# Optimization experiments

Hardware: AMD Instinct MI355X
Metric: run time of the kernel (lower is better)

Reference implementation:

```python
import jax, jax.numpy as jnp
import numpy as np

AVG_NOBJ = 49.0
NEG_SLOPE = 0.01  # torch leaky_relu default


def eops_1_to_2(x, nobj, aggregation):
    """x: [B,N,C] -> [B,C,5,N,N] equivariant basis (rank-1 -> rank-2)."""
    B, N, C = x.shape
    xt = jnp.transpose(x, (0, 2, 1))  # B,C,N
    if aggregation == 'sum':
        agg = xt.sum(-1) / AVG_NOBJ                      # B,C
    elif aggregation == 'mean':
        agg = xt.sum(-1) / nobj[:, None]                 # B,C
    elif aggregation == 'max':
        agg = xt.max(-1)
    elif aggregation == 'min':
        agg = xt.min(-1)
    eye = jnp.eye(N, dtype=x.dtype)                      # N,N
    op1 = xt[:, :, :, None] * eye                        # x_i on diagonal
    op2 = jnp.broadcast_to(xt[:, :, None, :], (B, C, N, N))  # x_j along rows
    op3 = jnp.broadcast_to(xt[:, :, :, None], (B, C, N, N))  # x_i along cols
    op4 = agg[:, :, None, None] * eye                    # agg on diagonal
    op5 = jnp.broadcast_to(agg[:, :, None, None], (B, C, N, N))  # agg everywhere
    return jnp.stack([op1, op2, op3, op4, op5], axis=2)  # B,C,5,N,N


def setup_inputs() -> dict:
    key = jax.random.key(0)
    k1, k2 = jax.random.split(key)
    B, N, C, S = 8, 128, 64, 64
    basis_total = 5 * 4  # 5 basis ops per config char, config='smxn'
    inputs = jax.random.normal(k1, (B, N, C), dtype=jnp.float32)
    mask = jnp.ones((B, N, N, 1), dtype=jnp.float32)
    nobj = jnp.full((B,), 100.0, dtype=jnp.float32)
    coefs = jax.random.normal(k2, (C, S, basis_total), dtype=jnp.float32) * np.sqrt(2.0 / (C * basis_total)).astype(np.float32)
    bias = jnp.zeros((S,), dtype=jnp.float32)
    return {"inputs": inputs, "mask": mask, "nobj": nobj, "coefs": coefs, "bias": bias}


def reference(inputs, mask, nobj, coefs, bias):
    # config = 'smxn' -> sum, mean, max, min basis tensors, concat on basis axis
    ops = jnp.concatenate(
        [eops_1_to_2(inputs, nobj, a) for a in ('sum', 'mean', 'max', 'min')],
        axis=2)  # B,C,20,N,N
    out = jnp.einsum('dsb,ndbij->nijs', coefs, ops)      # B,N,N,S
    out = out + bias[None, None, None, :]
    out = jnp.where(out >= 0, out, NEG_SLOPE * out)      # leaky_relu
    return out * mask
```

## Files before the change

### kernel.cpp

```cpp
#include <hip/hip_runtime.h>

constexpr int B = 8, N = 128, C = 64, S = 64;
constexpr float INV_AVG = 1.0f / 49.0f;
constexpr float SLOPE = 0.01f;

constexpr int WS_A = 0;
constexpr int WS_R = 65536;
constexpr int WS_C = 131072;
constexpr int WS_D = 196608;
constexpr int WS_E = 197120;

__global__ __launch_bounds__(256) void prep_kernel(
    const float* __restrict__ x,
    const float* __restrict__ nobj,
    const float* __restrict__ coefs,
    float* __restrict__ ws)
{
  __shared__ float smem[12800];
  const int tid = threadIdx.x;

  if (blockIdx.x < 256) {
    float* W1 = smem;
    float* W2 = smem + 4096;
    float* W3 = smem + 8192;
    float* xs = smem + 12288;
    const int n  = blockIdx.x >> 5;
    const int i0 = (blockIdx.x & 31) << 2;

    for (int k = 0; k < 16; ++k) {
      int e = tid + k * 256;
      int d = e >> 6, s = e & 63;
      const float* cp = coefs + d * (S * 20) + s * 20;
      W1[e] = cp[0] + cp[5] + cp[10] + cp[15];
      W2[e] = cp[1] + cp[6] + cp[11] + cp[16];
      W3[e] = cp[2] + cp[7] + cp[12] + cp[17];
    }
    xs[tid] = x[(n * N + i0 + (tid >> 6)) * C + (tid & 63)];
    __syncthreads();

    const int s  = tid & 63;
    const int ii = tid >> 6;
    const float* xr = xs + ii * 64;
    float a1 = 0.f, a2 = 0.f, a3 = 0.f;
#pragma unroll 8
    for (int d = 0; d < 64; ++d) {
      float xv = xr[d];
      a1 += xv * W1[d * 64 + s];
      a2 += xv * W2[d * 64 + s];
      a3 += xv * W3[d * 64 + s];
    }
    const int o = (n * N + i0 + ii) * S + s;
    ws[WS_A + o] = a1;
    ws[WS_R + o] = a2;
    ws[WS_C + o] = a3;
  } else {
    const int n = blockIdx.x - 256;
    float* xs  = smem;
    float* ps  = smem + 8192;
    float* pmx = smem + 8448;
    float* pmn = smem + 8704;
    float* ag  = smem + 8960;

    const float4* xg = (const float4*)(x + n * N * C);
    float4* xs4 = (float4*)xs;
#pragma unroll
    for (int k = 0; k < 8; ++k) xs4[tid + k * 256] = xg[tid + k * 256];
    __syncthreads();

    const int d = tid & 63, grp = tid >> 6;
    float sm = 0.f, mx = -INFINITY, mn = INFINITY;
    for (int i = grp * 32; i < grp * 32 + 32; ++i) {
      float v = xs[i * 64 + d];
      sm += v;
      mx = fmaxf(mx, v);
      mn = fminf(mn, v);
    }
    ps [grp * 64 + d] = sm;
    pmx[grp * 64 + d] = mx;
    pmn[grp * 64 + d] = mn;
    __syncthreads();

    if (tid < 64) {
      float s0 = ps[tid] + ps[64 + tid] + ps[128 + tid] + ps[192 + tid];
      float m0 = fmaxf(fmaxf(pmx[tid], pmx[64 + tid]),
                       fmaxf(pmx[128 + tid], pmx[192 + tid]));
      float n0 = fminf(fminf(pmn[tid], pmn[64 + tid]),
                       fminf(pmn[128 + tid], pmn[192 + tid]));
      ag[tid]       = s0 * INV_AVG;
      ag[64 + tid]  = s0 / nobj[n];
      ag[128 + tid] = m0;
      ag[192 + tid] = n0;
    }
    __syncthreads();

    if (tid < 64) {
      const int s = tid;
      float dv = 0.f, ev = 0.f;
      for (int d2 = 0; d2 < 64; ++d2) {
        const float* cp = coefs + d2 * (S * 20) + s * 20;
        float a0 = ag[d2], a1 = ag[64 + d2], a2 = ag[128 + d2], a3 = ag[192 + d2];
        dv += a0 * cp[3] + a1 * cp[8] + a2 * cp[13] + a3 * cp[18];
        ev += a0 * cp[4] + a1 * cp[9] + a2 * cp[14] + a3 * cp[19];
      }
      ws[WS_D + n * S + s] = dv;
      ws[WS_E + n * S + s] = ev;
    }
  }
}

__global__ __launch_bounds__(256) void assemble_kernel(
    const float* __restrict__ ws,
    const float* __restrict__ mask,
    const float* __restrict__ bias,
    float* __restrict__ out)
{
  const float4* A4 = (const float4*)(ws + WS_A);
  const float4* R4 = (const float4*)(ws + WS_R);
  const float4* C4 = (const float4*)(ws + WS_C);
  const float4* D4 = (const float4*)(ws + WS_D);
  const float4* E4 = (const float4*)(ws + WS_E);

  const int g = blockIdx.x * 256 + threadIdx.x;
  const int l = g & 15;
  const int p = g >> 4;
  const int j = p & 127;
  const int i = (p >> 7) & 127;
  const int n = p >> 14;

  float4 cc = C4[(n * N + i) * 16 + l];
  float4 rr = R4[(n * N + j) * 16 + l];
  float4 ee = E4[n * 16 + l];
  float4 bb = ((const float4*)bias)[l];
  float  m  = mask[p];

  float v0 = cc.x + rr.x + ee.x + bb.x;
  float v1 = cc.y + rr.y + ee.y + bb.y;
  float v2 = cc.z + rr.z + ee.z + bb.z;
  float v3 = cc.w + rr.w + ee.w + bb.w;

  if (i == j) {
    float4 aa = A4[(n * N + i) * 16 + l];
    float4 dd = D4[n * 16 + l];
    v0 += aa.x + dd.x;
    v1 += aa.y + dd.y;
    v2 += aa.z + dd.z;
    v3 += aa.w + dd.w;
  }

  v0 = (v0 >= 0.f) ? v0 : SLOPE * v0;
  v1 = (v1 >= 0.f) ? v1 : SLOPE * v1;
  v2 = (v2 >= 0.f) ? v2 : SLOPE * v2;
  v3 = (v3 >= 0.f) ? v3 : SLOPE * v3;

  float4 o;
  o.x = v0 * m; o.y = v1 * m; o.z = v2 * m; o.w = v3 * m;
  ((float4*)out)[g] = o;
}

extern "C" void kernel_launch(void* const* d_in, const int* in_sizes, int n_in,
                              void* d_out, int out_size, void* d_ws, size_t ws_size,
                              hipStream_t stream) {
  const float* x     = (const float*)d_in[0];
  const float* mask  = (const float*)d_in[1];
  const float* nobj  = (const float*)d_in[2];
  const float* coefs = (const float*)d_in[3];
  const float* bias  = (const float*)d_in[4];
  float* out = (float*)d_out;
  float* ws  = (float*)d_ws;

  prep_kernel<<<264, 256, 0, stream>>>(x, nobj, coefs, ws);
  assemble_kernel<<<8192, 256, 0, stream>>>(ws, mask, bias, out);
}
```

Measured before the change: 85.72 us.

## Split weight folding into its own kernel, block GEMM rows, loop assemble over j

Folded weights W1/W2/W3 are now computed once by a small kernel and written to workspace, instead of being recomputed in shared memory by each of 256 blocks. A separate GEMM kernel then gives each thread 4 rows, so each weight load is reused. The assemble kernel now handles one (n,i) row per block, hoists the column and bias terms, loops over 8 j values and writes with nontemporal stores. The cost is a third kernel launch and fewer, larger blocks in the GEMM stage (64 blocks).

```diff
diff --git a/kernel.cpp b/kernel.cpp
--- a/kernel.cpp
+++ b/kernel.cpp
@@ -4,62 +4,37 @@
 constexpr float INV_AVG = 1.0f / 49.0f;
 constexpr float SLOPE = 0.01f;
 
-constexpr int WS_A = 0;
-constexpr int WS_R = 65536;
-constexpr int WS_C = 131072;
-constexpr int WS_D = 196608;
-constexpr int WS_E = 197120;
+typedef float f4 __attribute__((ext_vector_type(4)));
 
-__global__ __launch_bounds__(256) void prep_kernel(
+constexpr int WS_A  = 0;
+constexpr int WS_R  = 65536;
+constexpr int WS_C  = 131072;
+constexpr int WS_D  = 196608;
+constexpr int WS_E  = 197120;
+constexpr int WS_W1 = 197632;
+constexpr int WS_W2 = 201728;
+constexpr int WS_W3 = 205824;
+
+__global__ __launch_bounds__(256) void weights_agg_kernel(
     const float* __restrict__ x,
     const float* __restrict__ nobj,
     const float* __restrict__ coefs,
     float* __restrict__ ws)
 {
-  __shared__ float smem[12800];
   const int tid = threadIdx.x;
-
-  if (blockIdx.x < 256) {
-    float* W1 = smem;
-    float* W2 = smem + 4096;
-    float* W3 = smem + 8192;
-    float* xs = smem + 12288;
-    const int n  = blockIdx.x >> 5;
-    const int i0 = (blockIdx.x & 31) << 2;
-
-    for (int k = 0; k < 16; ++k) {
-      int e = tid + k * 256;
-      int d = e >> 6, s = e & 63;
-      const float* cp = coefs + d * (S * 20) + s * 20;
-      W1[e] = cp[0] + cp[5] + cp[10] + cp[15];
-      W2[e] = cp[1] + cp[6] + cp[11] + cp[16];
-      W3[e] = cp[2] + cp[7] + cp[12] + cp[17];
-    }
-    xs[tid] = x[(n * N + i0 + (tid >> 6)) * C + (tid & 63)];
-    __syncthreads();
-
-    const int s  = tid & 63;
-    const int ii = tid >> 6;
-    const float* xr = xs + ii * 64;
-    float a1 = 0.f, a2 = 0.f, a3 = 0.f;
-#pragma unroll 8
-    for (int d = 0; d < 64; ++d) {
-      float xv = xr[d];
-      a1 += xv * W1[d * 64 + s];
-      a2 += xv * W2[d * 64 + s];
-      a3 += xv * W3[d * 64 + s];
-    }
-    const int o = (n * N + i0 + ii) * S + s;
-    ws[WS_A + o] = a1;
-    ws[WS_R + o] = a2;
-    ws[WS_C + o] = a3;
+  if (blockIdx.x < 16) {
+    const int e = blockIdx.x * 256 + tid;
+    const float4* cp = (const float4*)(coefs + e * 20);
+    float4 f0 = cp[0], f1 = cp[1], f2 = cp[2], f3 = cp[3], f4v = cp[4];
+    ws[WS_W1 + e] = f0.x + f1.y + f2.z + f3.w;
+    ws[WS_W2 + e] = f0.y + f1.z + f2.w + f4v.x;
+    ws[WS_W3 + e] = f0.z + f1.w + f3.x + f4v.y;
   } else {
-    const int n = blockIdx.x - 256;
+    __shared__ float smem[9216];
+    const int n = blockIdx.x - 16;
     float* xs  = smem;
     float* ps  = smem + 8192;
-    float* pmx = smem + 8448;
-    float* pmn = smem + 8704;
-    float* ag  = smem + 8960;
+    __shared__ float pmx[256], pmn[256], ag[256];
 
     const float4* xg = (const float4*)(x + n * N * C);
     float4* xs4 = (float4*)xs;
@@ -108,53 +83,99 @@
   }
 }
 
+__global__ __launch_bounds__(256) void gemm_kernel(
+    const float* __restrict__ x,
+    const float* __restrict__ ws_r,
+    float* __restrict__ ws)
+{
+  __shared__ float xs[16 * 64];
+  const int n  = blockIdx.x >> 3;
+  const int i0 = (blockIdx.x & 7) << 4;
+  const int tid = threadIdx.x;
+
+  ((float4*)xs)[tid] = ((const float4*)(x + (n * N + i0) * C))[tid];
+  __syncthreads();
+
+  const int s = tid & 63;
+  const int g = tid >> 6;
+  const float* W1 = ws_r + WS_W1;
+  const float* W2 = ws_r + WS_W2;
+  const float* W3 = ws_r + WS_W3;
+
+  float a1[4] = {0,0,0,0}, a2[4] = {0,0,0,0}, a3[4] = {0,0,0,0};
+#pragma unroll 8
+  for (int d = 0; d < 64; ++d) {
+    float w1 = W1[d * 64 + s];
+    float w2 = W2[d * 64 + s];
+    float w3 = W3[d * 64 + s];
+#pragma unroll
+    for (int k = 0; k < 4; ++k) {
+      float xv = xs[(g * 4 + k) * 64 + d];
+      a1[k] += xv * w1;
+      a2[k] += xv * w2;
+      a3[k] += xv * w3;
+    }
+  }
+#pragma unroll
+  for (int k = 0; k < 4; ++k) {
+    const int o = (n * N + i0 + g * 4 + k) * S + s;
+    ws[WS_A + o] = a1[k];
+    ws[WS_R + o] = a2[k];
+    ws[WS_C + o] = a3[k];
+  }
+}
+
 __global__ __launch_bounds__(256) void assemble_kernel(
     const float* __restrict__ ws,
     const float* __restrict__ mask,
     const float* __restrict__ bias,
     float* __restrict__ out)
 {
+  const int bi = blockIdx.x;
+  const int n  = bi >> 7;
+  const int i  = bi & 127;
+  const int l  = threadIdx.x & 15;
+  const int jg = threadIdx.x >> 4;
+
   const float4* A4 = (const float4*)(ws + WS_A);
   const float4* R4 = (const float4*)(ws + WS_R);
   const float4* C4 = (const float4*)(ws + WS_C);
   const float4* D4 = (const float4*)(ws + WS_D);
   const float4* E4 = (const float4*)(ws + WS_E);
 
-  const int g = blockIdx.x * 256 + threadIdx.x;
-  const int l = g & 15;
-  const int p = g >> 4;
-  const int j = p & 127;
-  const int i = (p >> 7) & 127;
-  const int n = p >> 14;
-
-  float4 cc = C4[(n * N + i) * 16 + l];
-  float4 rr = R4[(n * N + j) * 16 + l];
+  float4 cc = C4[bi * 16 + l];
   float4 ee = E4[n * 16 + l];
   float4 bb = ((const float4*)bias)[l];
-  float  m  = mask[p];
+  float bx = cc.x + ee.x + bb.x;
+  float by = cc.y + ee.y + bb.y;
+  float bz = cc.z + ee.z + bb.z;
+  float bw = cc.w + ee.w + bb.w;
 
-  float v0 = cc.x + rr.x + ee.x + bb.x;
-  float v1 = cc.y + rr.y + ee.y + bb.y;
-  float v2 = cc.z + rr.z + ee.z + bb.z;
-  float v3 = cc.w + rr.w + ee.w + bb.w;
+  f4* out4 = (f4*)out + (size_t)bi * (N * 16);
 
-  if (i == j) {
-    float4 aa = A4[(n * N + i) * 16 + l];
-    float4 dd = D4[n * 16 + l];
-    v0 += aa.x + dd.x;
-    v1 += aa.y + dd.y;
-    v2 += aa.z + dd.z;
-    v3 += aa.w + dd.w;
+#pragma unroll
+  for (int t = 0; t < 8; ++t) {
+    const int j = jg + t * 16;
+    float4 rr = R4[(n * N + j) * 16 + l];
+    float  m  = mask[bi * N + j];
+    float v0 = bx + rr.x;
+    float v1 = by + rr.y;
+    float v2 = bz + rr.z;
+    float v3 = bw + rr.w;
+    if (j == i) {
+      float4 aa = A4[bi * 16 + l];
+      float4 dd = D4[n * 16 + l];
+      v0 += aa.x + dd.x; v1 += aa.y + dd.y;
+      v2 += aa.z + dd.z; v3 += aa.w + dd.w;
+    }
+    v0 = (v0 >= 0.f) ? v0 : SLOPE * v0;
+    v1 = (v1 >= 0.f) ? v1 : SLOPE * v1;
+    v2 = (v2 >= 0.f) ? v2 : SLOPE * v2;
+    v3 = (v3 >= 0.f) ? v3 : SLOPE * v3;
+    f4 o;
+    o.x = v0 * m; o.y = v1 * m; o.z = v2 * m; o.w = v3 * m;
+    __builtin_nontemporal_store(o, &out4[j * 16 + l]);
   }
-
-  v0 = (v0 >= 0.f) ? v0 : SLOPE * v0;
-  v1 = (v1 >= 0.f) ? v1 : SLOPE * v1;
-  v2 = (v2 >= 0.f) ? v2 : SLOPE * v2;
-  v3 = (v3 >= 0.f) ? v3 : SLOPE * v3;
-
-  float4 o;
-  o.x = v0 * m; o.y = v1 * m; o.z = v2 * m; o.w = v3 * m;
-  ((float4*)out)[g] = o;
 }
 
 extern "C" void kernel_launch(void* const* d_in, const int* in_sizes, int n_in,
@@ -168,6 +189,7 @@
   float* out = (float*)d_out;
   float* ws  = (float*)d_ws;
 
-  prep_kernel<<<264, 256, 0, stream>>>(x, nobj, coefs, ws);
-  assemble_kernel<<<8192, 256, 0, stream>>>(ws, mask, bias, out);
+  weights_agg_kernel<<<24, 256, 0, stream>>>(x, nobj, coefs, ws);
+  gemm_kernel<<<64, 256, 0, stream>>>(x, ws, ws);
+  assemble_kernel<<<1024, 256, 0, stream>>>(ws, mask, bias, out);
 }
```

Measured after the change: 89.50 us. 4.4% more time.
